# Kernel tuning notes

Measured on AMD Instinct MI355X. Metric: run time of the kernel, lower is better.

## Reference

```python
import jax, jax.numpy as jnp
import numpy as np

IN_CH, OUT_CH, SCALE, K_UP, K_ENC, C_MID = 64, 32, 2, 3, 3, 64


def conv3d(x, w, b=None, pad=0):
    # x: (B,C,D,H,W), w: (O,I,kd,kh,kw)
    out = jax.lax.conv_general_dilated(
        x, w, window_strides=(1, 1, 1),
        padding=[(pad, pad)] * 3,
        dimension_numbers=("NCDHW", "OIDHW", "NCDHW"))
    if b is not None:
        out = out + b[None, :, None, None, None]
    return out


def pixel_shuffle3d(x, r):
    B, Cr3, D, H, W = x.shape
    C = Cr3 // r ** 3
    x = x.reshape(B, C, r, r, r, D, H, W)
    x = x.transpose(0, 1, 5, 2, 6, 3, 7, 4)  # B,C,D,r,H,r,W,r
    return x.reshape(B, C, D * r, H * r, W * r)


def setup_inputs() -> dict:
    key = jax.random.key(0)
    ks = jax.random.split(key, 6)
    B, C, D, H, W = 1, IN_CH, 32, 32, 32
    x = jax.random.normal(ks[0], (B, C, D, H, W), dtype=jnp.float32)
    Wc = jax.random.normal(ks[1], (C_MID, IN_CH, 1, 1, 1), dtype=jnp.float32) * 0.05
    bc = jax.random.normal(ks[2], (C_MID,), dtype=jnp.float32) * 0.05
    We = jax.random.normal(ks[3], (SCALE ** 3 * K_UP ** 3, C_MID, K_ENC, K_ENC, K_ENC), dtype=jnp.float32) * 0.05
    be = jax.random.normal(ks[4], (SCALE ** 3 * K_UP ** 3,), dtype=jnp.float32) * 0.05
    Wp = jax.random.normal(ks[5], (OUT_CH, IN_CH), dtype=jnp.float32) * 0.05
    return {"x": x, "Wc": Wc, "bc": bc, "We": We, "be": be, "Wp": Wp}


def reference(x, Wc, bc, We, be, Wp):
    B, C, D, H, W = x.shape
    s, k = SCALE, K_UP
    p = k // 2

    # kernel prediction branch
    w = conv3d(x, Wc, bc, pad=0)                 # (B, c_mid, D, H, W)
    w = conv3d(w, We, be, pad=K_ENC // 2)        # (B, s^3*k^3, D, H, W)
    w = pixel_shuffle3d(w, s)                    # (B, k^3, sD, sH, sW)
    w = jax.nn.softmax(w, axis=1)

    # gather k^3 neighborhoods (replicate padding); torch unfold order: depth slowest
    x_pad = jnp.pad(x, ((0, 0), (0, 0), (p, p), (p, p), (p, p)), mode="edge")
    patches = [x_pad[:, :, i:i + D, j:j + H, l:l + W]
               for i in range(k) for j in range(k) for l in range(k)]
    x_unf = jnp.stack(patches, axis=2)           # (B, C, k^3, D, H, W)

    # nearest-neighbor upsample of x_unf == each input cell serves its s^3 output cells;
    # fold that into the contraction instead of materializing (B,C,k^3,sD,sH,sW).
    wr = w.reshape(B, k ** 3, D, s, H, s, W, s)
    out = jnp.einsum("bcndhw,bndihjwl->bcdihjwl", x_unf, wr)
    out = out.reshape(B, C, D * s, H * s, W * s)

    # 1x1x1 projection (no bias)
    return jnp.einsum("oc,bcdhw->bodhw", Wp, out)
```

## Files before the change

### kernel.cpp

```cpp
#include <hip/hip_runtime.h>
#include <hip/hip_bf16.h>

#define V   32768
#define FV  262144
#define PD  34
#define PP  1156
#define NP  39304

#define NBA 308
#define NBX 256
#define NBW 216

typedef __attribute__((ext_vector_type(8))) short bf16x8;
typedef __attribute__((ext_vector_type(4))) float f32x4;
typedef __attribute__((ext_vector_type(4))) unsigned int u32x4;

__device__ __forceinline__ unsigned short f2bf(float f) {
    __hip_bfloat16 h = __float2bfloat16(f);
    return __builtin_bit_cast(unsigned short, h);
}
__device__ __forceinline__ float bf2f(unsigned short u) {
    unsigned int x = ((unsigned int)u) << 16;
    return __builtin_bit_cast(float, x);
}

__global__ __launch_bounds__(256) void kP(const float* __restrict__ x,
                                          const float* __restrict__ Wc,
                                          const float* __restrict__ bc,
                                          const float* __restrict__ Wp,
                                          const float* __restrict__ We,
                                          unsigned short* __restrict__ y1p,
                                          float* __restrict__ xp,
                                          unsigned short* __restrict__ Ab3) {
    __shared__ __align__(16) float sw[32 * 64];
    __shared__ float sbc[32];
    int tid = threadIdx.x;
    int bid = blockIdx.x;

    if (bid < NBA) {
        int vb = bid >> 1, half = bid & 1;
        for (int i = tid; i < 32 * 64; i += 256) sw[i] = Wc[half * 2048 + i];
        for (int i = tid; i < 32; i += 256) sbc[i] = bc[half * 32 + i];
        __syncthreads();

        int p = vb * 256 + tid;
        if (p >= NP) return;
        int pz = p / PP, rr = p - pz * PP;
        int py = rr / PD, px = rr - py * PD;
        unsigned short* dst = y1p + (size_t)p * 64 + half * 32;

        if (pz == 0 || pz == 33 || py == 0 || py == 33 || px == 0 || px == 33) {
            uint4 z4 = make_uint4(0, 0, 0, 0);
#pragma unroll
            for (int q = 0; q < 4; ++q) *(uint4*)(dst + q * 8) = z4;
            return;
        }
        int v = (pz - 1) * 1024 + (py - 1) * 32 + (px - 1);
        float xv[64];
#pragma unroll
        for (int c = 0; c < 64; ++c) xv[c] = x[c * V + v];

        unsigned int row[16];
        for (int m = 0; m < 32; m += 2) {
            float a0 = sbc[m], a1 = sbc[m + 1];
#pragma unroll
            for (int c4 = 0; c4 < 16; ++c4) {
                float4 w0 = *(const float4*)(sw + m * 64 + c4 * 4);
                float4 w1 = *(const float4*)(sw + (m + 1) * 64 + c4 * 4);
                a0 += w0.x * xv[c4 * 4] + w0.y * xv[c4 * 4 + 1] +
                      w0.z * xv[c4 * 4 + 2] + w0.w * xv[c4 * 4 + 3];
                a1 += w1.x * xv[c4 * 4] + w1.y * xv[c4 * 4 + 1] +
                      w1.z * xv[c4 * 4 + 2] + w1.w * xv[c4 * 4 + 3];
            }
            row[m >> 1] = (unsigned int)f2bf(a0) | ((unsigned int)f2bf(a1) << 16);
        }
#pragma unroll
        for (int q = 0; q < 4; ++q)
            *(uint4*)(dst + q * 8) =
                make_uint4(row[q * 4], row[q * 4 + 1], row[q * 4 + 2], row[q * 4 + 3]);

    } else if (bid < NBA + NBX) {
        int b2 = bid - NBA;
        int vb = b2 >> 1, half = b2 & 1;
        for (int i = tid; i < 16 * 64; i += 256) sw[i] = Wp[half * 1024 + i];
        __syncthreads();

        int v = vb * 256 + tid;
        float xv[64];
#pragma unroll
        for (int c = 0; c < 64; ++c) xv[c] = x[c * V + v];

        float pacc[16];
        for (int oc = 0; oc < 16; ++oc) {
            float acc = 0.f;
#pragma unroll
            for (int c4 = 0; c4 < 16; ++c4) {
                float4 w0 = *(const float4*)(sw + oc * 64 + c4 * 4);
                acc += w0.x * xv[c4 * 4] + w0.y * xv[c4 * 4 + 1] +
                       w0.z * xv[c4 * 4 + 2] + w0.w * xv[c4 * 4 + 3];
            }
            pacc[oc] = acc;
        }
#pragma unroll
        for (int q = 0; q < 4; ++q)
            *(float4*)(xp + (size_t)v * 32 + half * 16 + q * 4) =
                make_float4(pacc[q * 4], pacc[q * 4 + 1], pacc[q * 4 + 2], pacc[q * 4 + 3]);

    } else {
        int u = (bid - NBA - NBX) * 256 + tid;
        int lane = u & 63;
        int f = (u >> 6) & 7;
        int tmp = u >> 9;
        int tap = tmp % 27;
        int mblk = tmp / 27;
        int ks = f >> 2, i = f & 3;
        int m = mblk * 64 + i * 16 + (lane & 15);
        int c0 = (ks * 4 + (lane >> 4)) * 8;
        unsigned int pk[4];
#pragma unroll
        for (int p2 = 0; p2 < 4; ++p2) {
            unsigned int lo = 0, hi = 0;
            if (m < 216) {
                lo = f2bf(We[(m * 64 + c0 + 2 * p2) * 27 + tap]);
                hi = f2bf(We[(m * 64 + c0 + 2 * p2 + 1) * 27 + tap]);
            }
            pk[p2] = lo | (hi << 16);
        }
        ((uint4*)Ab3)[u] = make_uint4(pk[0], pk[1], pk[2], pk[3]);
    }
}

#define WAITV(N)                                                \
    { asm volatile("s_waitcnt vmcnt(" #N ")" ::: "memory");     \
      __builtin_amdgcn_sched_barrier(0); }

#define LOADA(AF, KT)                                                          \
    {                                                                          \
        unsigned long long _b0 = Abase + (unsigned long long)(KT) * 8192ull;   \
        unsigned long long _b1 = _b0 + 4096ull;                                \
        asm volatile("global_load_dwordx4 %0, %1, off"             : "=v"(AF[0]) : "v"(_b0) : "memory"); \
        asm volatile("global_load_dwordx4 %0, %1, off offset:1024" : "=v"(AF[1]) : "v"(_b0) : "memory"); \
        asm volatile("global_load_dwordx4 %0, %1, off offset:2048" : "=v"(AF[2]) : "v"(_b0) : "memory"); \
        asm volatile("global_load_dwordx4 %0, %1, off offset:3072" : "=v"(AF[3]) : "v"(_b0) : "memory"); \
        asm volatile("global_load_dwordx4 %0, %1, off"             : "=v"(AF[4]) : "v"(_b1) : "memory"); \
        asm volatile("global_load_dwordx4 %0, %1, off offset:1024" : "=v"(AF[5]) : "v"(_b1) : "memory"); \
        asm volatile("global_load_dwordx4 %0, %1, off offset:2048" : "=v"(AF[6]) : "v"(_b1) : "memory"); \
        asm volatile("global_load_dwordx4 %0, %1, off offset:3072" : "=v"(AF[7]) : "v"(_b1) : "memory"); \
    }

__global__ __launch_bounds__(256, 2) void kG(const unsigned short* __restrict__ Ab3,
                                             const unsigned short* __restrict__ y1p,
                                             const float* __restrict__ be,
                                             unsigned short* __restrict__ y2) {
    __shared__ unsigned short sH[240 * 64];
    int tid = threadIdx.x, lane = tid & 63, wid = tid >> 6;
    int bidx = blockIdx.x;
    int bw = bidx & 3, by = (bidx >> 2) & 7, bz = bidx >> 5;

    for (int it = 0; it < 8; ++it) {
        int u = it * 256 + tid;
        if (u < 1920) {
            int q = u & 7, p = u >> 3;
            int hx = p % 10, t2 = p / 10;
            int hy = t2 % 6, hz = t2 / 6;
            size_t src = ((size_t)(bz * 2 + hz) * PP + (by * 4 + hy) * PD + (bw * 8 + hx)) * 64
                         + q * 8;
            uint4 val = *(const uint4*)(y1p + src);
            *(uint4*)((char*)sH + (p * 8 + (q ^ (p & 7))) * 16) = val;
        }
    }

    int p0[4], vv[4];
#pragma unroll
    for (int j = 0; j < 4; ++j) {
        int n = j * 16 + (lane & 15);
        int wz = n >> 5, wy = (n >> 3) & 3, wx = n & 7;
        p0[j] = wz * 60 + wy * 10 + wx;
        vv[j] = (bz * 2 + wz) * 1024 + (by * 4 + wy) * 32 + bw * 8 + wx;
    }

    f32x4 acc[4][4] = {};
    __syncthreads();

    unsigned long long Abase = (unsigned long long)(const void*)Ab3 +
                               (unsigned long long)wid * 27ull * 8192ull +
                               (unsigned long long)lane * 16ull;
    u32x4 afA[8], afB[8], afC[8];
    LOADA(afA, 0);
    LOADA(afB, 1);
    LOADA(afC, 2);

#define COMPUTE(KT, AF)                                                       \
    {                                                                         \
        int dz = (KT) / 9, rem = (KT) - dz * 9;                               \
        int dy = rem / 3, dx = rem - dy * 3;                                  \
        int pofs = dz * 60 + dy * 10 + dx;                                    \
        _Pragma("unroll")                                                     \
        for (int ks = 0; ks < 2; ++ks) {                                      \
            bf16x8 b[4];                                                      \
            int cc = ks * 4 + (lane >> 4);                                    \
            _Pragma("unroll")                                                 \
            for (int j = 0; j < 4; ++j) {                                     \
                int p = p0[j] + pofs;                                         \
                b[j] = *(const bf16x8*)(sH + p * 64 + (cc ^ (p & 7)) * 8);    \
            }                                                                 \
            _Pragma("unroll")                                                 \
            for (int i = 0; i < 4; ++i) {                                     \
                bf16x8 a = __builtin_bit_cast(bf16x8, AF[ks * 4 + i]);        \
                _Pragma("unroll")                                             \
                for (int j = 0; j < 4; ++j)                                   \
                    acc[i][j] = __builtin_amdgcn_mfma_f32_16x16x32_bf16(      \
                        a, b[j], acc[i][j], 0, 0, 0);                         \
            }                                                                 \
        }                                                                     \
    }

    for (int kt = 0; kt <= 21; kt += 3) {
        WAITV(16); COMPUTE(kt,     afA); LOADA(afA, kt + 3);
        WAITV(16); COMPUTE(kt + 1, afB); LOADA(afB, kt + 4);
        WAITV(16); COMPUTE(kt + 2, afC); LOADA(afC, kt + 5);
    }
    WAITV(16); COMPUTE(24, afA);
    WAITV(8);  COMPUTE(25, afB);
    WAITV(0);  COMPUTE(26, afC);
#undef COMPUTE

#pragma unroll
    for (int i = 0; i < 4; ++i) {
        int mb = wid * 64 + i * 16 + (lane >> 4) * 4;
#pragma unroll
        for (int r = 0; r < 4; ++r) {
            int m = mb + r;
            if (m < 216) {
                float bv = be[m];
#pragma unroll
                for (int j = 0; j < 4; ++j)
                    y2[(size_t)m * V + vv[j]] = f2bf(acc[i][j][r] + bv);
            }
        }
    }
}
#undef WAITV
#undef LOADA

__global__ __launch_bounds__(512) void kC(const unsigned short* __restrict__ y2,
                                          const float* __restrict__ xp,
                                          float* __restrict__ out) {
    __shared__ float  slog[8][27][32];
    __shared__ float4 sxp[9][32][8];
    int t = threadIdx.x;
    int bid = blockIdx.x;
    int d = bid >> 5, h = bid & 31;

    for (int idx = t; idx < 6912; idx += 512) {
        int g = idx / 864, r = idx - g * 864;
        int tp = r >> 5, w = r & 31;
        slog[g][tp][w] = bf2f(y2[(size_t)(tp * 8 + g) * V + d * 1024 + h * 32 + w]);
    }
    for (int idx = t; idx < 2304; idx += 512) {
        int zy = idx >> 8, r = idx & 255;
        int xx = r >> 3, q = r & 7;
        int zi = zy / 3, yi = zy - zi * 3;
        int zz = min(max(d + zi - 1, 0), 31);
        int yy = min(max(h + yi - 1, 0), 31);
        sxp[zy][xx][q ^ (xx & 7)] =
            *(const float4*)(xp + (size_t)(zz * 1024 + yy * 32 + xx) * 32 + q * 4);
    }
    __syncthreads();

    if (t < 256) {
        int g = t >> 5, w = t & 31;
        float lg[27];
#pragma unroll
        for (int tp = 0; tp < 27; ++tp) lg[tp] = slog[g][tp][w];
        float m = lg[0];
#pragma unroll
        for (int tp = 1; tp < 27; ++tp) m = fmaxf(m, lg[tp]);
        float s = 0.f;
#pragma unroll
        for (int tp = 0; tp < 27; ++tp) { lg[tp] = __expf(lg[tp] - m); s += lg[tp]; }
        float inv = 1.f / s;
#pragma unroll
        for (int tp = 0; tp < 27; ++tp) slog[g][tp][w] = lg[tp] * inv;
    }
    __syncthreads();

    {
        int sh = t >> 8, g = (t >> 5) & 7, w = t & 31;
        float acc[4][4] = {};
#pragma unroll
        for (int zy = 0; zy < 9; ++zy) {
#pragma unroll
            for (int dx = 0; dx < 3; ++dx) {
                int tap = zy * 3 + dx;
                int xx = min(max(w + dx - 1, 0), 31);
                float4 xv = sxp[zy][xx][g ^ (xx & 7)];
                float wn[4];
#pragma unroll
                for (int s = 0; s < 4; ++s) wn[s] = slog[sh * 4 + s][tap][w];
#pragma unroll
                for (int s = 0; s < 4; ++s) {
                    acc[s][0] += wn[s] * xv.x;
                    acc[s][1] += wn[s] * xv.y;
                    acc[s][2] += wn[s] * xv.z;
                    acc[s][3] += wn[s] * xv.w;
                }
            }
        }

        int fzb = 2 * d, fyb = 2 * h;
#pragma unroll
        for (int spl = 0; spl < 2; ++spl) {
            int sp = sh * 2 + spl;
            int i = sp >> 1, j = sp & 1;
            size_t ob = (size_t)(fzb + i) * 4096 + (size_t)(fyb + j) * 64 + 2 * w;
#pragma unroll
            for (int k = 0; k < 4; ++k) {
                float2 v2 = make_float2(acc[2 * spl][k], acc[2 * spl + 1][k]);
                *(float2*)(out + (size_t)(g * 4 + k) * FV + ob) = v2;
            }
        }
    }
}

extern "C" void kernel_launch(void* const* d_in, const int* in_sizes, int n_in,
                              void* d_out, int out_size, void* d_ws, size_t ws_size,
                              hipStream_t stream) {
    const float* x  = (const float*)d_in[0];
    const float* Wc = (const float*)d_in[1];
    const float* bc = (const float*)d_in[2];
    const float* We = (const float*)d_in[3];
    const float* be = (const float*)d_in[4];
    const float* Wp = (const float*)d_in[5];
    float* out = (float*)d_out;

    float* ws = (float*)d_ws;
    float* xp = ws;
    unsigned short* y2  = (unsigned short*)(xp + (size_t)32 * V);
    unsigned short* Ab3 = y2 + (size_t)216 * V;
    unsigned short* y1p = Ab3 + (size_t)55296 * 8;

    kP<<<NBA + NBX + NBW, 256, 0, stream>>>(x, Wc, bc, Wp, We, y1p, xp, Ab3);
    kG<<<512, 256, 0, stream>>>(Ab3, y1p, be, y2);
    kC<<<1024, 512, 0, stream>>>(y2, xp, out);
}
```

Baseline: 83.13 us.

## Fuse projection into conv branch and double kG voxel tile per block

The 1x1 Wp projection now runs inside the Wc conv blocks of the prep kernel. It reuses the already loaded x values instead of launching separate blocks that reload x. The main MFMA kernel doubles its depth tile, so each block covers 128 voxels with a larger shared-memory halo and holds accumulators for 8 voxel groups. That halves the A-weight global loads per voxel. The pipeline drops from triple to double buffering and occupancy drops to one block per CU with only 256 blocks. This risks poorer latency hiding and uneven load across the CUs.

```diff
diff --git a/kernel.cpp b/kernel.cpp
--- a/kernel.cpp
+++ b/kernel.cpp
@@ -8,7 +8,6 @@
 #define NP  39304
 
 #define NBA 308
-#define NBX 256
 #define NBW 216
 
 typedef __attribute__((ext_vector_type(8))) short bf16x8;
@@ -33,6 +32,7 @@
                                           float* __restrict__ xp,
                                           unsigned short* __restrict__ Ab3) {
     __shared__ __align__(16) float sw[32 * 64];
+    __shared__ __align__(16) float swp[16 * 64];
     __shared__ float sbc[32];
     int tid = threadIdx.x;
     int bid = blockIdx.x;
@@ -40,6 +40,7 @@
     if (bid < NBA) {
         int vb = bid >> 1, half = bid & 1;
         for (int i = tid; i < 32 * 64; i += 256) sw[i] = Wc[half * 2048 + i];
+        for (int i = tid; i < 16 * 64; i += 256) swp[i] = Wp[half * 1024 + i];
         for (int i = tid; i < 32; i += 256) sbc[i] = bc[half * 32 + i];
         __syncthreads();
 
@@ -79,23 +80,12 @@
             *(uint4*)(dst + q * 8) =
                 make_uint4(row[q * 4], row[q * 4 + 1], row[q * 4 + 2], row[q * 4 + 3]);
 
-    } else if (bid < NBA + NBX) {
-        int b2 = bid - NBA;
-        int vb = b2 >> 1, half = b2 & 1;
-        for (int i = tid; i < 16 * 64; i += 256) sw[i] = Wp[half * 1024 + i];
-        __syncthreads();
-
-        int v = vb * 256 + tid;
-        float xv[64];
-#pragma unroll
-        for (int c = 0; c < 64; ++c) xv[c] = x[c * V + v];
-
         float pacc[16];
         for (int oc = 0; oc < 16; ++oc) {
             float acc = 0.f;
 #pragma unroll
             for (int c4 = 0; c4 < 16; ++c4) {
-                float4 w0 = *(const float4*)(sw + oc * 64 + c4 * 4);
+                float4 w0 = *(const float4*)(swp + oc * 64 + c4 * 4);
                 acc += w0.x * xv[c4 * 4] + w0.y * xv[c4 * 4 + 1] +
                        w0.z * xv[c4 * 4 + 2] + w0.w * xv[c4 * 4 + 3];
             }
@@ -107,7 +97,7 @@
                 make_float4(pacc[q * 4], pacc[q * 4 + 1], pacc[q * 4 + 2], pacc[q * 4 + 3]);
 
     } else {
-        int u = (bid - NBA - NBX) * 256 + tid;
+        int u = (bid - NBA) * 256 + tid;
         int lane = u & 63;
         int f = (u >> 6) & 7;
         int tmp = u >> 9;
@@ -148,47 +138,46 @@
         asm volatile("global_load_dwordx4 %0, %1, off offset:3072" : "=v"(AF[7]) : "v"(_b1) : "memory"); \
     }
 
-__global__ __launch_bounds__(256, 2) void kG(const unsigned short* __restrict__ Ab3,
+__global__ __launch_bounds__(256, 1) void kG(const unsigned short* __restrict__ Ab3,
                                              const unsigned short* __restrict__ y1p,
                                              const float* __restrict__ be,
                                              unsigned short* __restrict__ y2) {
-    __shared__ unsigned short sH[240 * 64];
+    __shared__ unsigned short sH[360 * 64];
     int tid = threadIdx.x, lane = tid & 63, wid = tid >> 6;
     int bidx = blockIdx.x;
     int bw = bidx & 3, by = (bidx >> 2) & 7, bz = bidx >> 5;
 
-    for (int it = 0; it < 8; ++it) {
+    for (int it = 0; it < 12; ++it) {
         int u = it * 256 + tid;
-        if (u < 1920) {
+        if (u < 2880) {
             int q = u & 7, p = u >> 3;
             int hx = p % 10, t2 = p / 10;
             int hy = t2 % 6, hz = t2 / 6;
-            size_t src = ((size_t)(bz * 2 + hz) * PP + (by * 4 + hy) * PD + (bw * 8 + hx)) * 64
+            size_t src = ((size_t)(bz * 4 + hz) * PP + (by * 4 + hy) * PD + (bw * 8 + hx)) * 64
                          + q * 8;
             uint4 val = *(const uint4*)(y1p + src);
             *(uint4*)((char*)sH + (p * 8 + (q ^ (p & 7))) * 16) = val;
         }
     }
 
-    int p0[4], vv[4];
-#pragma unroll
-    for (int j = 0; j < 4; ++j) {
+    int p0[8], vv[8];
+#pragma unroll
+    for (int j = 0; j < 8; ++j) {
         int n = j * 16 + (lane & 15);
         int wz = n >> 5, wy = (n >> 3) & 3, wx = n & 7;
         p0[j] = wz * 60 + wy * 10 + wx;
-        vv[j] = (bz * 2 + wz) * 1024 + (by * 4 + wy) * 32 + bw * 8 + wx;
-    }
-
-    f32x4 acc[4][4] = {};
+        vv[j] = (bz * 4 + wz) * 1024 + (by * 4 + wy) * 32 + bw * 8 + wx;
+    }
+
+    f32x4 acc[4][8] = {};
     __syncthreads();
 
     unsigned long long Abase = (unsigned long long)(const void*)Ab3 +
                                (unsigned long long)wid * 27ull * 8192ull +
                                (unsigned long long)lane * 16ull;
-    u32x4 afA[8], afB[8], afC[8];
+    u32x4 afA[8], afB[8];
     LOADA(afA, 0);
     LOADA(afB, 1);
-    LOADA(afC, 2);
 
 #define COMPUTE(KT, AF)                                                       \
     {                                                                         \
@@ -197,32 +186,28 @@
         int pofs = dz * 60 + dy * 10 + dx;                                    \
         _Pragma("unroll")                                                     \
         for (int ks = 0; ks < 2; ++ks) {                                      \
-            bf16x8 b[4];                                                      \
             int cc = ks * 4 + (lane >> 4);                                    \
             _Pragma("unroll")                                                 \
-            for (int j = 0; j < 4; ++j) {                                     \
+            for (int j = 0; j < 8; ++j) {                                     \
                 int p = p0[j] + pofs;                                         \
-                b[j] = *(const bf16x8*)(sH + p * 64 + (cc ^ (p & 7)) * 8);    \
-            }                                                                 \
-            _Pragma("unroll")                                                 \
-            for (int i = 0; i < 4; ++i) {                                     \
-                bf16x8 a = __builtin_bit_cast(bf16x8, AF[ks * 4 + i]);        \
+                bf16x8 b = *(const bf16x8*)(sH + p * 64 + (cc ^ (p & 7)) * 8);\
                 _Pragma("unroll")                                             \
-                for (int j = 0; j < 4; ++j)                                   \
+                for (int i = 0; i < 4; ++i) {                                 \
+                    bf16x8 a = __builtin_bit_cast(bf16x8, AF[ks * 4 + i]);    \
                     acc[i][j] = __builtin_amdgcn_mfma_f32_16x16x32_bf16(      \
-                        a, b[j], acc[i][j], 0, 0, 0);                         \
+                        a, b, acc[i][j], 0, 0, 0);                            \
+                }                                                             \
             }                                                                 \
         }                                                                     \
     }
 
-    for (int kt = 0; kt <= 21; kt += 3) {
-        WAITV(16); COMPUTE(kt,     afA); LOADA(afA, kt + 3);
-        WAITV(16); COMPUTE(kt + 1, afB); LOADA(afB, kt + 4);
-        WAITV(16); COMPUTE(kt + 2, afC); LOADA(afC, kt + 5);
-    }
-    WAITV(16); COMPUTE(24, afA);
-    WAITV(8);  COMPUTE(25, afB);
-    WAITV(0);  COMPUTE(26, afC);
+    for (int kt = 0; kt <= 24; kt += 2) {
+        WAITV(8); COMPUTE(kt, afA);
+        if (kt + 2 < 27) LOADA(afA, kt + 2);
+        WAITV(8); COMPUTE(kt + 1, afB);
+        if (kt + 3 < 27) LOADA(afB, kt + 3);
+    }
+    WAITV(0); COMPUTE(26, afA);
 #undef COMPUTE
 
 #pragma unroll
@@ -234,7 +219,7 @@
             if (m < 216) {
                 float bv = be[m];
 #pragma unroll
-                for (int j = 0; j < 4; ++j)
+                for (int j = 0; j < 8; ++j)
                     y2[(size_t)m * V + vv[j]] = f2bf(acc[i][j][r] + bv);
             }
         }
@@ -340,7 +325,7 @@
     unsigned short* Ab3 = y2 + (size_t)216 * V;
     unsigned short* y1p = Ab3 + (size_t)55296 * 8;
 
-    kP<<<NBA + NBX + NBW, 256, 0, stream>>>(x, Wc, bc, Wp, We, y1p, xp, Ab3);
-    kG<<<512, 256, 0, stream>>>(Ab3, y1p, be, y2);
+    kP<<<NBA + NBW, 256, 0, stream>>>(x, Wc, bc, Wp, We, y1p, xp, Ab3);
+    kG<<<256, 256, 0, stream>>>(Ab3, y1p, be, y2);
     kC<<<1024, 512, 0, stream>>>(y2, xp, out);
 }
```

Result: slower. 99.67 us (+19.9%).

## Fuse Wp projection into conv1 blocks and split combine kernel across sub-positions

Applied to the files above, without the earlier changes.

The separate kP block range that recomputed the 64-channel x vector for the 1x1 projection is removed. Its work is folded into the conv1 blocks, which already load the same x values, so x is read once and the grid shrinks. The final combine kernel gains a second grid dimension so each block handles only half of the 8 sub-voxel logit groups. This lowers per-thread accumulators and shared memory and doubles block count, at the cost of loading the shared xp neighbourhood twice.

```diff
diff --git a/kernel.cpp b/kernel.cpp
--- a/kernel.cpp
+++ b/kernel.cpp
@@ -8,7 +8,6 @@
 #define NP  39304
 
 #define NBA 308
-#define NBX 256
 #define NBW 216
 
 typedef __attribute__((ext_vector_type(8))) short bf16x8;
@@ -33,6 +32,7 @@
                                           float* __restrict__ xp,
                                           unsigned short* __restrict__ Ab3) {
     __shared__ __align__(16) float sw[32 * 64];
+    __shared__ __align__(16) float swp[16 * 64];
     __shared__ float sbc[32];
     int tid = threadIdx.x;
     int bid = blockIdx.x;
@@ -40,6 +40,7 @@
     if (bid < NBA) {
         int vb = bid >> 1, half = bid & 1;
         for (int i = tid; i < 32 * 64; i += 256) sw[i] = Wc[half * 2048 + i];
+        for (int i = tid; i < 16 * 64; i += 256) swp[i] = Wp[half * 1024 + i];
         for (int i = tid; i < 32; i += 256) sbc[i] = bc[half * 32 + i];
         __syncthreads();
 
@@ -79,23 +80,12 @@
             *(uint4*)(dst + q * 8) =
                 make_uint4(row[q * 4], row[q * 4 + 1], row[q * 4 + 2], row[q * 4 + 3]);
 
-    } else if (bid < NBA + NBX) {
-        int b2 = bid - NBA;
-        int vb = b2 >> 1, half = b2 & 1;
-        for (int i = tid; i < 16 * 64; i += 256) sw[i] = Wp[half * 1024 + i];
-        __syncthreads();
-
-        int v = vb * 256 + tid;
-        float xv[64];
-#pragma unroll
-        for (int c = 0; c < 64; ++c) xv[c] = x[c * V + v];
-
         float pacc[16];
         for (int oc = 0; oc < 16; ++oc) {
             float acc = 0.f;
 #pragma unroll
             for (int c4 = 0; c4 < 16; ++c4) {
-                float4 w0 = *(const float4*)(sw + oc * 64 + c4 * 4);
+                float4 w0 = *(const float4*)(swp + oc * 64 + c4 * 4);
                 acc += w0.x * xv[c4 * 4] + w0.y * xv[c4 * 4 + 1] +
                        w0.z * xv[c4 * 4 + 2] + w0.w * xv[c4 * 4 + 3];
             }
@@ -107,7 +97,7 @@
                 make_float4(pacc[q * 4], pacc[q * 4 + 1], pacc[q * 4 + 2], pacc[q * 4 + 3]);
 
     } else {
-        int u = (bid - NBA - NBX) * 256 + tid;
+        int u = (bid - NBA) * 256 + tid;
         int lane = u & 63;
         int f = (u >> 6) & 7;
         int tmp = u >> 9;
@@ -246,16 +236,17 @@
 __global__ __launch_bounds__(512) void kC(const unsigned short* __restrict__ y2,
                                           const float* __restrict__ xp,
                                           float* __restrict__ out) {
-    __shared__ float  slog[8][27][32];
+    __shared__ float  slog[4][27][32];
     __shared__ float4 sxp[9][32][8];
     int t = threadIdx.x;
     int bid = blockIdx.x;
+    int sh = blockIdx.y;
     int d = bid >> 5, h = bid & 31;
 
-    for (int idx = t; idx < 6912; idx += 512) {
+    for (int idx = t; idx < 3456; idx += 512) {
         int g = idx / 864, r = idx - g * 864;
         int tp = r >> 5, w = r & 31;
-        slog[g][tp][w] = bf2f(y2[(size_t)(tp * 8 + g) * V + d * 1024 + h * 32 + w]);
+        slog[g][tp][w] = bf2f(y2[(size_t)(tp * 8 + sh * 4 + g) * V + d * 1024 + h * 32 + w]);
     }
     for (int idx = t; idx < 2304; idx += 512) {
         int zy = idx >> 8, r = idx & 255;
@@ -268,7 +259,7 @@
     }
     __syncthreads();
 
-    if (t < 256) {
+    if (t < 128) {
         int g = t >> 5, w = t & 31;
         float lg[27];
 #pragma unroll
@@ -286,8 +277,8 @@
     __syncthreads();
 
     {
-        int sh = t >> 8, g = (t >> 5) & 7, w = t & 31;
-        float acc[4][4] = {};
+        int spl = t >> 8, g = (t >> 5) & 7, w = t & 31;
+        float acc[2][4] = {};
 #pragma unroll
         for (int zy = 0; zy < 9; ++zy) {
 #pragma unroll
@@ -295,30 +286,22 @@
                 int tap = zy * 3 + dx;
                 int xx = min(max(w + dx - 1, 0), 31);
                 float4 xv = sxp[zy][xx][g ^ (xx & 7)];
-                float wn[4];
-#pragma unroll
-                for (int s = 0; s < 4; ++s) wn[s] = slog[sh * 4 + s][tap][w];
-#pragma unroll
-                for (int s = 0; s < 4; ++s) {
-                    acc[s][0] += wn[s] * xv.x;
-                    acc[s][1] += wn[s] * xv.y;
-                    acc[s][2] += wn[s] * xv.z;
-                    acc[s][3] += wn[s] * xv.w;
-                }
-            }
-        }
-
-        int fzb = 2 * d, fyb = 2 * h;
-#pragma unroll
-        for (int spl = 0; spl < 2; ++spl) {
-            int sp = sh * 2 + spl;
-            int i = sp >> 1, j = sp & 1;
-            size_t ob = (size_t)(fzb + i) * 4096 + (size_t)(fyb + j) * 64 + 2 * w;
-#pragma unroll
-            for (int k = 0; k < 4; ++k) {
-                float2 v2 = make_float2(acc[2 * spl][k], acc[2 * spl + 1][k]);
-                *(float2*)(out + (size_t)(g * 4 + k) * FV + ob) = v2;
-            }
+                float w0 = slog[spl * 2 + 0][tap][w];
+                float w1 = slog[spl * 2 + 1][tap][w];
+                acc[0][0] += w0 * xv.x;  acc[0][1] += w0 * xv.y;
+                acc[0][2] += w0 * xv.z;  acc[0][3] += w0 * xv.w;
+                acc[1][0] += w1 * xv.x;  acc[1][1] += w1 * xv.y;
+                acc[1][2] += w1 * xv.z;  acc[1][3] += w1 * xv.w;
+            }
+        }
+
+        int sp = sh * 2 + spl;
+        int i = sp >> 1, j = sp & 1;
+        size_t ob = (size_t)(2 * d + i) * 4096 + (size_t)(2 * h + j) * 64 + 2 * w;
+#pragma unroll
+        for (int k = 0; k < 4; ++k) {
+            float2 v2 = make_float2(acc[0][k], acc[1][k]);
+            *(float2*)(out + (size_t)(g * 4 + k) * FV + ob) = v2;
         }
     }
 }
@@ -340,7 +323,7 @@
     unsigned short* Ab3 = y2 + (size_t)216 * V;
     unsigned short* y1p = Ab3 + (size_t)55296 * 8;
 
-    kP<<<NBA + NBX + NBW, 256, 0, stream>>>(x, Wc, bc, Wp, We, y1p, xp, Ab3);
+    kP<<<NBA + NBW, 256, 0, stream>>>(x, Wc, bc, Wp, We, y1p, xp, Ab3);
     kG<<<512, 256, 0, stream>>>(Ab3, y1p, be, y2);
-    kC<<<1024, 512, 0, stream>>>(y2, xp, out);
-}
+    kC<<<dim3(1024, 2), 512, 0, stream>>>(y2, xp, out);
+}
```

After: 94.86 us. +14.1%, slower.
